# Optimization experiments

Hardware: AMD Instinct MI355X
Metric: run time of the kernel (lower is better)

Reference implementation:

```python
import jax, jax.numpy as jnp
import numpy as np

B, T, C, H, MAX_LEN = 16, 512, 1024, 16, 512
D = C // H  # head_dim = 64

def setup_inputs() -> dict:
    key = jax.random.key(0)
    ks = jax.random.split(key, 10)
    s = 1.0 / np.sqrt(C)
    return {
        "x": jax.random.normal(ks[0], (B, T, C), dtype=jnp.float32),
        "Wq": jax.random.normal(ks[1], (C, C), dtype=jnp.float32) * s,
        "bq": jnp.zeros((C,), dtype=jnp.float32),
        "Wk": jax.random.normal(ks[2], (C, C), dtype=jnp.float32) * s,
        "bk": jnp.zeros((C,), dtype=jnp.float32),
        "Wv": jax.random.normal(ks[3], (C, C), dtype=jnp.float32) * s,
        "bv": jnp.zeros((C,), dtype=jnp.float32),
        "Wo": jax.random.normal(ks[4], (C, C), dtype=jnp.float32) * s,
        "bo": jnp.zeros((C,), dtype=jnp.float32),
        "rel_pos_bias": jax.random.normal(ks[5], (H, MAX_LEN, MAX_LEN), dtype=jnp.float32) * 0.02,
    }

def reference(x, Wq, bq, Wk, bk, Wv, bv, Wo, bo, rel_pos_bias):
    scale = 1.0 / jnp.sqrt(jnp.float32(D))
    # projections (torch Linear: x @ W.T + b), reshape to (B,H,T,D)
    def proj(W, b):
        return (x @ W.T + b).reshape(B, T, H, D).transpose(0, 2, 1, 3)
    q, k, v = proj(Wq, bq), proj(Wk, bk), proj(Wv, bv)
    attn = jnp.einsum('bhtd,bhsd->bhts', q, k) * scale  # (B,H,T,T)
    attn = attn + rel_pos_bias[None, :, :T, :T]
    causal = jnp.triu(jnp.ones((T, T), dtype=bool), k=1)
    attn = jnp.where(causal[None, None], -jnp.inf, attn)
    attn = jax.nn.softmax(attn, axis=-1)  # dropout p=0 (eval) -> identity
    out = jnp.einsum('bhts,bhsd->bhtd', attn, v)
    out = out.transpose(0, 2, 1, 3).reshape(B, T, C)
    return out @ Wo.T + bo
```

## Files before the change

kernel.cpp:

```cpp
#include <hip/hip_runtime.h>
#include <stdint.h>
#include <math.h>

#define DEV static __device__ __forceinline__

typedef __attribute__((ext_vector_type(8))) __bf16 bf16x8;
typedef __attribute__((ext_vector_type(4))) float f32x4;
typedef unsigned short u16;

DEV u16 f2b(float f) {
  union { float f; uint32_t u; } x; x.f = f;
  uint32_t r = x.u + 0x7fffu + ((x.u >> 16) & 1u);
  return (u16)(r >> 16);
}

DEV uint32_t pk2(float a, float b) {
  return (uint32_t)f2b(a) | ((uint32_t)f2b(b) << 16);
}

DEV float b2f_lo(uint32_t u) { return __uint_as_float(u << 16); }
DEV float b2f_hi(uint32_t u) { return __uint_as_float(u & 0xffff0000u); }

DEV void glds16(const void* g, void* l) {
  __builtin_amdgcn_global_load_lds(
      (const __attribute__((address_space(1))) void*)g,
      (__attribute__((address_space(3))) void*)l, 16, 0, 0);
}

DEV f32x4 mfma16(bf16x8 a, bf16x8 b, f32x4 c) {
  return __builtin_amdgcn_mfma_f32_16x16x32_bf16(a, b, c, 0, 0, 0);
}

#define BAR() __builtin_amdgcn_s_barrier()
#define WAIT_LGKM()                                      \
  {                                                      \
    asm volatile("s_waitcnt lgkmcnt(0)" ::: "memory");   \
    __builtin_amdgcn_sched_barrier(0);                   \
  }
#define WAIT_VM3() asm volatile("s_waitcnt vmcnt(3)" ::: "memory")
#define WAIT_VM0() asm volatile("s_waitcnt vmcnt(0)" ::: "memory")

__global__ __launch_bounds__(256) void cvt_all(
    const float* __restrict__ x, const float* __restrict__ Wq,
    const float* __restrict__ Wk, const float* __restrict__ Wv,
    const float* __restrict__ Wo, const float* __restrict__ bias,
    u16* __restrict__ xb, u16* __restrict__ wqkv, u16* __restrict__ wo,
    u16* __restrict__ biasb) {
  size_t i = ((size_t)blockIdx.x * 256 + threadIdx.x) * 4;
  const float* s;
  u16* d;
  size_t off;
  float scale = 1.0f;
  if (i < 8388608)        { s = x;  d = xb;             off = i; }
  else if (i < 9437184)   { s = Wq; d = wqkv;           off = i - 8388608; }
  else if (i < 10485760)  { s = Wk; d = wqkv + 1048576; off = i - 9437184; }
  else if (i < 11534336)  { s = Wv; d = wqkv + 2097152; off = i - 10485760; }
  else if (i < 12582912)  { s = Wo; d = wo;             off = i - 11534336; }
  else { s = bias; d = biasb; off = i - 12582912; scale = 1.44269504f; }
  float4 v = *(const float4*)(s + off);
  ushort4 o;
  o.x = f2b(v.x * scale); o.y = f2b(v.y * scale);
  o.z = f2b(v.z * scale); o.w = f2b(v.w * scale);
  *(ushort4*)(d + off) = o;
}


DEV void stage_slot(const u16* A, const u16* Bw, int m0, int n0, int col,
                    int wave, int srow, int scol, u16* slotA, u16* slotB) {
  const u16* srcA = A + (size_t)(m0 + wave * 32 + srow) * 1024 + col + scol;
  glds16(srcA, slotA + wave * 1024);
  glds16(srcA + (size_t)16 * 1024, slotA + wave * 1024 + 512);
  glds16(Bw + (size_t)(n0 + wave * 16 + srow) * 1024 + col + scol,
         slotB + wave * 512);
}

DEV void load_frags(const u16* Rbase, const u16* Cbase, int wr, int wc,
                    int c16, int swz, bf16x8 rf[4], bf16x8 cf[4]) {
#pragma unroll
  for (int i = 0; i < 4; ++i)
    rf[i] = *(const bf16x8*)&Rbase[(wr * 64 + i * 16 + c16) * 32 + swz];
#pragma unroll
  for (int i = 0; i < 4; ++i)
    cf[i] = *(const bf16x8*)&Cbase[(wc * 64 + i * 16 + c16) * 32 + swz];
}

DEV void mfma_all(bf16x8 rf[4], bf16x8 cf[4], f32x4 acc[4][4]) {
#pragma unroll
  for (int i = 0; i < 4; ++i)
#pragma unroll
    for (int j = 0; j < 4; ++j) acc[i][j] = mfma16(rf[i], cf[j], acc[i][j]);
}

DEV void gemm_core(const u16* A, const u16* Bw, int m0, int n0, bool vblk,
                   int wave, int lane, u16 (*lsA)[8192], u16 (*lsB)[4096],
                   f32x4 acc[4][4]) {
  int q16 = lane >> 4, c16 = lane & 15;
  int wm = wave >> 1, wn = wave & 1;
  int wr = vblk ? wn : wm, wc = vblk ? wm : wn;
  int srow = lane >> 2;
  int scol = ((lane & 3) ^ ((lane >> 3) & 3)) * 8;
  int swz = (q16 ^ ((c16 >> 1) & 3)) * 8;

  stage_slot(A, Bw, m0, n0, 0, wave, srow, scol, lsA[0], lsB[0]);
  stage_slot(A, Bw, m0, n0, 32, wave, srow, scol, lsA[1], lsB[1]);
  WAIT_VM3();
  BAR();

#pragma unroll
  for (int g = 0; g < 32; ++g) {
    const int slot = g % 3;
    const u16* Rb = vblk ? &lsB[slot][0] : &lsA[slot][0];
    const u16* Cb = vblk ? &lsA[slot][0] : &lsB[slot][0];
    bf16x8 rf[4], cf[4];
    load_frags(Rb, Cb, wr, wc, c16, swz, rf, cf);
    if (g < 30)
      stage_slot(A, Bw, m0, n0, (g + 2) * 32, wave, srow, scol,
                 lsA[(g + 2) % 3], lsB[(g + 2) % 3]);
    BAR();
    WAIT_LGKM();
    __builtin_amdgcn_s_setprio(1);
    mfma_all(rf, cf, acc);
    __builtin_amdgcn_s_setprio(0);
    if (g < 30) { WAIT_VM3(); } else if (g == 30) { WAIT_VM0(); }
    BAR();
  }
}

__global__ __launch_bounds__(512, 4) void gemm_qkv(
    const u16* __restrict__ A, const u16* __restrict__ Bw,
    const float* __restrict__ bq, const float* __restrict__ bk,
    const float* __restrict__ bv,
    u16* __restrict__ qo, u16* __restrict__ ko, u16* __restrict__ vto) {
  __shared__ u16 lsA[3][8192];
  __shared__ u16 lsB[3][4096];
  int tid = threadIdx.x, wave = tid >> 6, lane = tid & 63;
  int q16 = lane >> 4, c16 = lane & 15;
  int m0 = blockIdx.y * 256, n0 = blockIdx.x * 128;
  int wm = wave >> 1, wn = wave & 1;
  const bool vblk = (n0 >= 2048);

  f32x4 acc[4][4];
#pragma unroll
  for (int i = 0; i < 4; ++i)
#pragma unroll
    for (int j = 0; j < 4; ++j) acc[i][j] = (f32x4)0.0f;

  gemm_core(A, Bw, m0, n0, vblk, wave, lane, lsA, lsB, acc);

  if (!vblk) {
#pragma unroll
    for (int mt = 0; mt < 4; ++mt) {
#pragma unroll
      for (int nt = 0; nt < 4; ++nt) {
        int n = n0 + wn * 64 + nt * 16 + c16;
        int which = n >> 10;
        int nl = n & 1023;
        int hh = nl >> 6, d = nl & 63;
        float bias = (which == 0 ? bq : bk)[nl];
        u16* dst = (which == 0 ? qo : ko);
#pragma unroll
        for (int r = 0; r < 4; ++r) {
          int m = m0 + wm * 64 + mt * 16 + q16 * 4 + r;
          int b = m >> 9, t = m & 511;
          size_t bh = (size_t)b * 16 + hh;
          dst[(bh * 512 + t) * 72 + d] = f2b(acc[mt][nt][r] + bias);
        }
      }
    }
  } else {
#pragma unroll
    for (int it = 0; it < 4; ++it) {
      int nbase = n0 + wn * 64 + it * 16 + q16 * 4;
      float4 bvv = *(const float4*)(bv + (nbase & 1023));
#pragma unroll
      for (int jt = 0; jt < 4; ++jt) {
        int m = m0 + wm * 64 + jt * 16 + c16;
        int b = m >> 9, t = m & 511;
        size_t bh4 = ((size_t)b * 16) * 4;
#pragma unroll
        for (int r = 0; r < 4; ++r) {
          int nl = (nbase + r) & 1023;
          int hh = nl >> 6, d = nl & 63;
          float bias = ((const float*)&bvv)[r];
          vto[((bh4 + (size_t)hh * 4 + (t >> 7)) * 64 + d) * 136 + (t & 127)] =
              f2b(acc[it][jt][r] + bias);
        }
      }
    }
  }
}

__global__ __launch_bounds__(256, 3) void attn_kernel(
    const u16* __restrict__ qglob, const u16* __restrict__ kglob,
    const u16* __restrict__ vtglob, const u16* __restrict__ biasb,
    u16* __restrict__ og) {
  __shared__ u16 lsK[128 * 72];
  __shared__ u16 lsV[64 * 136];
  __shared__ u16 lsP[4 * 32 * 72];

  int tid = threadIdx.x, wave = tid >> 6, lane = tid & 63;
  int q16 = lane >> 4, c16 = lane & 15;
  u16* lsPw = lsP + wave * (32 * 72);

  int p = blockIdx.x;
  int bx, bh, bx2 = -1, bh2 = 0;
  if (p < 256)      { bx = 3; bh = p; }
  else if (p < 512) { bx = 2; bh = p - 256; bx2 = 0; bh2 = p - 256; }
  else              { int q = p - 512; bx = 1; bh = 2 * q; bx2 = 1; bh2 = 2 * q + 1; }

  for (;;) {
    int b = bh >> 4, h = bh & 15;
    int q0 = bx * 128;

    const u16* qbase = qglob + (size_t)bh * (512 * 72) + (size_t)q0 * 72;
    const u16* kbase = kglob + (size_t)bh * (512 * 72);
    const u16* vbase = vtglob + (size_t)bh * 4 * (64 * 136);

    for (int i = wave; i < 18; i += 4)
      glds16(qbase + (size_t)i * 512 + lane * 8, lsK + i * 512);
    __syncthreads();
    bf16x8 qf[2][2];
#pragma unroll
    for (int nt = 0; nt < 2; ++nt)
#pragma unroll
      for (int ks = 0; ks < 2; ++ks)
        qf[nt][ks] = *(const bf16x8*)&lsK[(wave * 32 + nt * 16 + c16) * 72 +
                                          ks * 32 + q16 * 8];

    f32x4 oacc[2][4];
#pragma unroll
    for (int i = 0; i < 2; ++i)
#pragma unroll
      for (int j = 0; j < 4; ++j) oacc[i][j] = (f32x4)0.0f;
    float mold[2] = {-INFINITY, -INFINITY};
    float lsum[2] = {0.0f, 0.0f};
    const float SCL = 0.18033688f;

    for (int st = 0; st <= bx; ++st) {
      bool diag = (st == bx);
      __syncthreads();
      const u16* kt = kbase + (size_t)st * (128 * 72);
      for (int i = wave; i < 18; i += 4)
        glds16(kt + (size_t)i * 512 + lane * 8, lsK + i * 512);
      const u16* vt = vbase + (size_t)st * (64 * 136);
      for (int i = wave; i < 17; i += 4)
        glds16(vt + (size_t)i * 512 + lane * 8, lsV + i * 512);

      uint2 ub[2][8];
#pragma unroll
      for (int nt = 0; nt < 2; ++nt) {
        int qgl = q0 + wave * 32 + nt * 16 + c16;
        const u16* bp =
            biasb + ((size_t)h * 512 + qgl) * 512 + st * 128 + q16 * 4;
#pragma unroll
        for (int mt = 0; mt < 8; ++mt) ub[nt][mt] = *(const uint2*)(bp + mt * 16);
      }
      __syncthreads();

      f32x4 sa[8][2];
#pragma unroll
      for (int mt = 0; mt < 8; ++mt) {
        sa[mt][0] = (f32x4)0.0f;
        sa[mt][1] = (f32x4)0.0f;
      }
      int mtmax = diag ? 2 * wave + 2 : 8;
#pragma unroll
      for (int mt = 0; mt < 8; ++mt) {
        if (mt < mtmax) {
#pragma unroll
          for (int ks = 0; ks < 2; ++ks) {
            bf16x8 kf =
                *(const bf16x8*)&lsK[(mt * 16 + c16) * 72 + ks * 32 + q16 * 8];
            sa[mt][0] = mfma16(kf, qf[0][ks], sa[mt][0]);
            sa[mt][1] = mfma16(kf, qf[1][ks], sa[mt][1]);
          }
        }
      }

      float alpha[2];
#pragma unroll
      for (int nt = 0; nt < 2; ++nt) {
#pragma unroll
        for (int mt = 0; mt < 8; ++mt) {
          uint32_t lo = ub[nt][mt].x, hi = ub[nt][mt].y;
          f32x4 bv;
          bv[0] = b2f_lo(lo); bv[1] = b2f_hi(lo);
          bv[2] = b2f_lo(hi); bv[3] = b2f_hi(hi);
          sa[mt][nt] = sa[mt][nt] * SCL + bv;
        }
        if (diag) {
#pragma unroll
          for (int mt = 0; mt < 8; ++mt) {
            int d0 = mt * 16 + q16 * 4 - wave * 32 - nt * 16 - c16;
#pragma unroll
            for (int r = 0; r < 4; ++r)
              if (d0 + r > 0) sa[mt][nt][r] = -INFINITY;
          }
        }
        f32x4 m4 = sa[0][nt];
#pragma unroll
        for (int mt = 1; mt < 8; ++mt) {
          f32x4 v = sa[mt][nt];
          m4[0] = fmaxf(m4[0], v[0]); m4[1] = fmaxf(m4[1], v[1]);
          m4[2] = fmaxf(m4[2], v[2]); m4[3] = fmaxf(m4[3], v[3]);
        }
        float mx = fmaxf(fmaxf(m4[0], m4[1]), fmaxf(m4[2], m4[3]));
        mx = fmaxf(mx, __shfl_xor(mx, 16));
        mx = fmaxf(mx, __shfl_xor(mx, 32));
        float mnew = fmaxf(mold[nt], mx);
        alpha[nt] = exp2f(mold[nt] - mnew);
        mold[nt] = mnew;
        f32x4 s4 = (f32x4)0.0f;
#pragma unroll
        for (int mt = 0; mt < 8; ++mt) {
          f32x4 pq;
          pq[0] = exp2f(sa[mt][nt][0] - mnew);
          pq[1] = exp2f(sa[mt][nt][1] - mnew);
          pq[2] = exp2f(sa[mt][nt][2] - mnew);
          pq[3] = exp2f(sa[mt][nt][3] - mnew);
          sa[mt][nt] = pq;
          s4 += pq;
        }
        float ss = (s4[0] + s4[1]) + (s4[2] + s4[3]);
        ss += __shfl_xor(ss, 16);
        ss += __shfl_xor(ss, 32);
        lsum[nt] = lsum[nt] * alpha[nt] + ss;
      }

#pragma unroll
      for (int mo = 0; mo < 2; ++mo) {
        f32x4 av;
#pragma unroll
        for (int r = 0; r < 4; ++r) av[r] = __shfl(alpha[mo], q16 * 4 + r);
#pragma unroll
        for (int dt = 0; dt < 4; ++dt) oacc[mo][dt] *= av;
      }

      int G = diag ? wave + 1 : 4;
#pragma unroll
      for (int hf = 0; hf < 2; ++hf) {
        if (hf * 2 < G) {
#pragma unroll
          for (int nt = 0; nt < 2; ++nt)
#pragma unroll
            for (int mt4 = 0; mt4 < 4; ++mt4) {
              f32x4 pv = sa[hf * 4 + mt4][nt];
              uint2 w;
              w.x = pk2(pv[0], pv[1]);
              w.y = pk2(pv[2], pv[3]);
              *(uint2*)&lsPw[(nt * 16 + c16) * 72 + mt4 * 16 + q16 * 4] = w;
            }
#pragma unroll
          for (int ksh = 0; ksh < 2; ++ksh) {
            if (hf * 2 + ksh < G) {
              bf16x8 pf0 =
                  *(const bf16x8*)&lsPw[c16 * 72 + ksh * 32 + q16 * 8];
              bf16x8 pf1 =
                  *(const bf16x8*)&lsPw[(16 + c16) * 72 + ksh * 32 + q16 * 8];
#pragma unroll
              for (int dt = 0; dt < 4; ++dt) {
                bf16x8 vf = *(const bf16x8*)&lsV[(dt * 16 + c16) * 136 +
                                                 hf * 64 + ksh * 32 + q16 * 8];
                oacc[0][dt] = mfma16(pf0, vf, oacc[0][dt]);
                oacc[1][dt] = mfma16(pf1, vf, oacc[1][dt]);
              }
            }
          }
        }
      }
    }

#pragma unroll
    for (int mo = 0; mo < 2; ++mo) {
      f32x4 lv;
#pragma unroll
      for (int r = 0; r < 4; ++r) lv[r] = __shfl(lsum[mo], q16 * 4 + r);
#pragma unroll
      for (int r = 0; r < 4; ++r) {
        int tg = q0 + wave * 32 + mo * 16 + q16 * 4 + r;
        float inv = 1.0f / lv[r];
#pragma unroll
        for (int dt = 0; dt < 4; ++dt)
          og[((size_t)b * 512 + tg) * 1024 + h * 64 + dt * 16 + c16] =
              f2b(oacc[mo][dt][r] * inv);
      }
    }

    if (bx2 < 0) break;
    __syncthreads();
    bx = bx2; bh = bh2; bx2 = -1;
  }
}

__global__ __launch_bounds__(512, 4) void gemm_out(
    const u16* __restrict__ A, const u16* __restrict__ W,
    const float* __restrict__ bo, float* __restrict__ out) {
  __shared__ u16 lsA[3][8192];
  __shared__ u16 lsB[3][4096];
  int tid = threadIdx.x, wave = tid >> 6, lane = tid & 63;
  int q16 = lane >> 4, c16 = lane & 15;
  int m0 = blockIdx.y * 256, n0 = blockIdx.x * 128;
  int wm = wave >> 1, wn = wave & 1;

  f32x4 acc[4][4];
#pragma unroll
  for (int i = 0; i < 4; ++i)
#pragma unroll
    for (int j = 0; j < 4; ++j) acc[i][j] = (f32x4)0.0f;

  gemm_core(A, W, m0, n0, false, wave, lane, lsA, lsB, acc);

#pragma unroll
  for (int mt = 0; mt < 4; ++mt) {
#pragma unroll
    for (int nt = 0; nt < 4; ++nt) {
      int n = n0 + wn * 64 + nt * 16 + c16;
      float bias = bo[n];
#pragma unroll
      for (int r = 0; r < 4; ++r) {
        int m = m0 + wm * 64 + mt * 16 + q16 * 4 + r;
        out[(size_t)m * 1024 + n] = acc[mt][nt][r] + bias;
      }
    }
  }
}

extern "C" void kernel_launch(void* const* d_in, const int* in_sizes, int n_in,
                              void* d_out, int out_size, void* d_ws, size_t ws_size,
                              hipStream_t stream) {
  const float* x    = (const float*)d_in[0];
  const float* Wq   = (const float*)d_in[1];
  const float* bq   = (const float*)d_in[2];
  const float* Wk   = (const float*)d_in[3];
  const float* bk   = (const float*)d_in[4];
  const float* Wv   = (const float*)d_in[5];
  const float* bv   = (const float*)d_in[6];
  const float* Wo   = (const float*)d_in[7];
  const float* bo   = (const float*)d_in[8];
  const float* bias = (const float*)d_in[9];
  float* out = (float*)d_out;

  const size_t MB = 1u << 20;
  char* ws = (char*)d_ws;
  u16* xb    = (u16*)(ws);
  u16* wqkv  = (u16*)(ws + 16 * MB);
  u16* wo    = (u16*)(ws + 22 * MB);
  u16* biasb = (u16*)(ws + 24 * MB);
  u16* qb    = (u16*)(ws + 32 * MB);
  u16* kb    = (u16*)(ws + 50 * MB);
  u16* vtb   = (u16*)(ws + 68 * MB);
  u16* ab    = xb;

  cvt_all<<<16384, 256, 0, stream>>>(x, Wq, Wk, Wv, Wo, bias,
                                     xb, wqkv, wo, biasb);
  gemm_qkv<<<dim3(24, 32), 512, 0, stream>>>(xb, wqkv, bq, bk, bv, qb, kb, vtb);
  attn_kernel<<<dim3(640), 256, 0, stream>>>(qb, kb, vtb, biasb, ab);
  gemm_out<<<dim3(8, 32), 512, 0, stream>>>(ab, wo, bo, out);
}
```

Before: 269.1 us.

## Split attention query tile across eight waves of 16 rows each

Attention blocks grow from 4 to 8 waves, and each wave now owns 16 query rows instead of 32. Per-wave register state (scores, accumulators, bias loads) halves, and the causal diagonal tile is masked at finer granularity, so less MFMA work is wasted on masked entries. The per-wave P staging buffer shrinks and its row stride changes to 68. The cost is that each K/V fragment read from LDS is reused by only one query tile instead of two, which doubles LDS read traffic per unit of MFMA work.

```diff
diff --git a/kernel.cpp b/kernel.cpp
--- a/kernel.cpp
+++ b/kernel.cpp
@@ -190,17 +190,17 @@
   }
 }
 
-__global__ __launch_bounds__(256, 3) void attn_kernel(
+__global__ __launch_bounds__(512, 6) void attn_kernel(
     const u16* __restrict__ qglob, const u16* __restrict__ kglob,
     const u16* __restrict__ vtglob, const u16* __restrict__ biasb,
     u16* __restrict__ og) {
   __shared__ u16 lsK[128 * 72];
   __shared__ u16 lsV[64 * 136];
-  __shared__ u16 lsP[4 * 32 * 72];
+  __shared__ u16 lsP[8 * 16 * 68];
 
   int tid = threadIdx.x, wave = tid >> 6, lane = tid & 63;
   int q16 = lane >> 4, c16 = lane & 15;
-  u16* lsPw = lsP + wave * (32 * 72);
+  u16* lsPw = lsP + wave * (16 * 68);
 
   int p = blockIdx.x;
   int bx, bh, bx2 = -1, bh2 = 0;
@@ -216,54 +216,45 @@
     const u16* kbase = kglob + (size_t)bh * (512 * 72);
     const u16* vbase = vtglob + (size_t)bh * 4 * (64 * 136);
 
-    for (int i = wave; i < 18; i += 4)
+    for (int i = wave; i < 18; i += 8)
       glds16(qbase + (size_t)i * 512 + lane * 8, lsK + i * 512);
     __syncthreads();
-    bf16x8 qf[2][2];
-#pragma unroll
-    for (int nt = 0; nt < 2; ++nt)
-#pragma unroll
-      for (int ks = 0; ks < 2; ++ks)
-        qf[nt][ks] = *(const bf16x8*)&lsK[(wave * 32 + nt * 16 + c16) * 72 +
-                                          ks * 32 + q16 * 8];
-
-    f32x4 oacc[2][4];
-#pragma unroll
-    for (int i = 0; i < 2; ++i)
-#pragma unroll
-      for (int j = 0; j < 4; ++j) oacc[i][j] = (f32x4)0.0f;
-    float mold[2] = {-INFINITY, -INFINITY};
-    float lsum[2] = {0.0f, 0.0f};
+    bf16x8 qf[2];
+#pragma unroll
+    for (int ks = 0; ks < 2; ++ks)
+      qf[ks] = *(const bf16x8*)&lsK[(wave * 16 + c16) * 72 + ks * 32 + q16 * 8];
+
+    f32x4 oacc[4];
+#pragma unroll
+    for (int j = 0; j < 4; ++j) oacc[j] = (f32x4)0.0f;
+    float mold = -INFINITY;
+    float lsum = 0.0f;
     const float SCL = 0.18033688f;
 
     for (int st = 0; st <= bx; ++st) {
       bool diag = (st == bx);
       __syncthreads();
       const u16* kt = kbase + (size_t)st * (128 * 72);
-      for (int i = wave; i < 18; i += 4)
+      for (int i = wave; i < 18; i += 8)
         glds16(kt + (size_t)i * 512 + lane * 8, lsK + i * 512);
       const u16* vt = vbase + (size_t)st * (64 * 136);
-      for (int i = wave; i < 17; i += 4)
+      for (int i = wave; i < 17; i += 8)
         glds16(vt + (size_t)i * 512 + lane * 8, lsV + i * 512);
 
-      uint2 ub[2][8];
-#pragma unroll
-      for (int nt = 0; nt < 2; ++nt) {
-        int qgl = q0 + wave * 32 + nt * 16 + c16;
+      uint2 ub[8];
+      {
+        int qgl = q0 + wave * 16 + c16;
         const u16* bp =
             biasb + ((size_t)h * 512 + qgl) * 512 + st * 128 + q16 * 4;
 #pragma unroll
-        for (int mt = 0; mt < 8; ++mt) ub[nt][mt] = *(const uint2*)(bp + mt * 16);
+        for (int mt = 0; mt < 8; ++mt) ub[mt] = *(const uint2*)(bp + mt * 16);
       }
       __syncthreads();
 
-      f32x4 sa[8][2];
-#pragma unroll
-      for (int mt = 0; mt < 8; ++mt) {
-        sa[mt][0] = (f32x4)0.0f;
-        sa[mt][1] = (f32x4)0.0f;
-      }
-      int mtmax = diag ? 2 * wave + 2 : 8;
+      f32x4 sa[8];
+#pragma unroll
+      for (int mt = 0; mt < 8; ++mt) sa[mt] = (f32x4)0.0f;
+      int mtmax = diag ? wave + 1 : 8;
 #pragma unroll
       for (int mt = 0; mt < 8; ++mt) {
         if (mt < mtmax) {
@@ -271,98 +262,87 @@
           for (int ks = 0; ks < 2; ++ks) {
             bf16x8 kf =
                 *(const bf16x8*)&lsK[(mt * 16 + c16) * 72 + ks * 32 + q16 * 8];
-            sa[mt][0] = mfma16(kf, qf[0][ks], sa[mt][0]);
-            sa[mt][1] = mfma16(kf, qf[1][ks], sa[mt][1]);
+            sa[mt] = mfma16(kf, qf[ks], sa[mt]);
           }
         }
       }
 
-      float alpha[2];
-#pragma unroll
-      for (int nt = 0; nt < 2; ++nt) {
+#pragma unroll
+      for (int mt = 0; mt < 8; ++mt) {
+        uint32_t lo = ub[mt].x, hi = ub[mt].y;
+        f32x4 bv;
+        bv[0] = b2f_lo(lo); bv[1] = b2f_hi(lo);
+        bv[2] = b2f_lo(hi); bv[3] = b2f_hi(hi);
+        sa[mt] = sa[mt] * SCL + bv;
+      }
+      if (diag) {
 #pragma unroll
         for (int mt = 0; mt < 8; ++mt) {
-          uint32_t lo = ub[nt][mt].x, hi = ub[nt][mt].y;
-          f32x4 bv;
-          bv[0] = b2f_lo(lo); bv[1] = b2f_hi(lo);
-          bv[2] = b2f_lo(hi); bv[3] = b2f_hi(hi);
-          sa[mt][nt] = sa[mt][nt] * SCL + bv;
+          int d0 = mt * 16 + q16 * 4 - wave * 16 - c16;
+#pragma unroll
+          for (int r = 0; r < 4; ++r)
+            if (d0 + r > 0) sa[mt][r] = -INFINITY;
         }
-        if (diag) {
-#pragma unroll
-          for (int mt = 0; mt < 8; ++mt) {
-            int d0 = mt * 16 + q16 * 4 - wave * 32 - nt * 16 - c16;
-#pragma unroll
-            for (int r = 0; r < 4; ++r)
-              if (d0 + r > 0) sa[mt][nt][r] = -INFINITY;
-          }
-        }
-        f32x4 m4 = sa[0][nt];
-#pragma unroll
-        for (int mt = 1; mt < 8; ++mt) {
-          f32x4 v = sa[mt][nt];
-          m4[0] = fmaxf(m4[0], v[0]); m4[1] = fmaxf(m4[1], v[1]);
-          m4[2] = fmaxf(m4[2], v[2]); m4[3] = fmaxf(m4[3], v[3]);
-        }
-        float mx = fmaxf(fmaxf(m4[0], m4[1]), fmaxf(m4[2], m4[3]));
-        mx = fmaxf(mx, __shfl_xor(mx, 16));
-        mx = fmaxf(mx, __shfl_xor(mx, 32));
-        float mnew = fmaxf(mold[nt], mx);
-        alpha[nt] = exp2f(mold[nt] - mnew);
-        mold[nt] = mnew;
-        f32x4 s4 = (f32x4)0.0f;
-#pragma unroll
-        for (int mt = 0; mt < 8; ++mt) {
-          f32x4 pq;
-          pq[0] = exp2f(sa[mt][nt][0] - mnew);
-          pq[1] = exp2f(sa[mt][nt][1] - mnew);
-          pq[2] = exp2f(sa[mt][nt][2] - mnew);
-          pq[3] = exp2f(sa[mt][nt][3] - mnew);
-          sa[mt][nt] = pq;
-          s4 += pq;
-        }
-        float ss = (s4[0] + s4[1]) + (s4[2] + s4[3]);
-        ss += __shfl_xor(ss, 16);
-        ss += __shfl_xor(ss, 32);
-        lsum[nt] = lsum[nt] * alpha[nt] + ss;
-      }
-
-#pragma unroll
-      for (int mo = 0; mo < 2; ++mo) {
+      }
+      f32x4 m4 = sa[0];
+#pragma unroll
+      for (int mt = 1; mt < 8; ++mt) {
+        f32x4 v = sa[mt];
+        m4[0] = fmaxf(m4[0], v[0]); m4[1] = fmaxf(m4[1], v[1]);
+        m4[2] = fmaxf(m4[2], v[2]); m4[3] = fmaxf(m4[3], v[3]);
+      }
+      float mx = fmaxf(fmaxf(m4[0], m4[1]), fmaxf(m4[2], m4[3]));
+      mx = fmaxf(mx, __shfl_xor(mx, 16));
+      mx = fmaxf(mx, __shfl_xor(mx, 32));
+      float mnew = fmaxf(mold, mx);
+      float alpha = exp2f(mold - mnew);
+      mold = mnew;
+      f32x4 s4 = (f32x4)0.0f;
+#pragma unroll
+      for (int mt = 0; mt < 8; ++mt) {
+        f32x4 pq;
+        pq[0] = exp2f(sa[mt][0] - mnew);
+        pq[1] = exp2f(sa[mt][1] - mnew);
+        pq[2] = exp2f(sa[mt][2] - mnew);
+        pq[3] = exp2f(sa[mt][3] - mnew);
+        sa[mt] = pq;
+        s4 += pq;
+      }
+      float ss = (s4[0] + s4[1]) + (s4[2] + s4[3]);
+      ss += __shfl_xor(ss, 16);
+      ss += __shfl_xor(ss, 32);
+      lsum = lsum * alpha + ss;
+
+      {
         f32x4 av;
 #pragma unroll
-        for (int r = 0; r < 4; ++r) av[r] = __shfl(alpha[mo], q16 * 4 + r);
-#pragma unroll
-        for (int dt = 0; dt < 4; ++dt) oacc[mo][dt] *= av;
-      }
-
-      int G = diag ? wave + 1 : 4;
+        for (int r = 0; r < 4; ++r) av[r] = __shfl(alpha, q16 * 4 + r);
+#pragma unroll
+        for (int dt = 0; dt < 4; ++dt) oacc[dt] *= av;
+      }
+
+      int G = diag ? (wave >> 1) + 1 : 4;
 #pragma unroll
       for (int hf = 0; hf < 2; ++hf) {
         if (hf * 2 < G) {
 #pragma unroll
-          for (int nt = 0; nt < 2; ++nt)
-#pragma unroll
-            for (int mt4 = 0; mt4 < 4; ++mt4) {
-              f32x4 pv = sa[hf * 4 + mt4][nt];
-              uint2 w;
-              w.x = pk2(pv[0], pv[1]);
-              w.y = pk2(pv[2], pv[3]);
-              *(uint2*)&lsPw[(nt * 16 + c16) * 72 + mt4 * 16 + q16 * 4] = w;
-            }
+          for (int mt4 = 0; mt4 < 4; ++mt4) {
+            f32x4 pv = sa[hf * 4 + mt4];
+            uint2 w;
+            w.x = pk2(pv[0], pv[1]);
+            w.y = pk2(pv[2], pv[3]);
+            *(uint2*)&lsPw[c16 * 68 + mt4 * 16 + q16 * 4] = w;
+          }
 #pragma unroll
           for (int ksh = 0; ksh < 2; ++ksh) {
             if (hf * 2 + ksh < G) {
-              bf16x8 pf0 =
-                  *(const bf16x8*)&lsPw[c16 * 72 + ksh * 32 + q16 * 8];
-              bf16x8 pf1 =
-                  *(const bf16x8*)&lsPw[(16 + c16) * 72 + ksh * 32 + q16 * 8];
+              bf16x8 pf =
+                  *(const bf16x8*)&lsPw[c16 * 68 + ksh * 32 + q16 * 8];
 #pragma unroll
               for (int dt = 0; dt < 4; ++dt) {
                 bf16x8 vf = *(const bf16x8*)&lsV[(dt * 16 + c16) * 136 +
                                                  hf * 64 + ksh * 32 + q16 * 8];
-                oacc[0][dt] = mfma16(pf0, vf, oacc[0][dt]);
-                oacc[1][dt] = mfma16(pf1, vf, oacc[1][dt]);
+                oacc[dt] = mfma16(pf, vf, oacc[dt]);
               }
             }
           }
@@ -370,19 +350,18 @@
       }
     }
 
-#pragma unroll
-    for (int mo = 0; mo < 2; ++mo) {
+    {
       f32x4 lv;
 #pragma unroll
-      for (int r = 0; r < 4; ++r) lv[r] = __shfl(lsum[mo], q16 * 4 + r);
+      for (int r = 0; r < 4; ++r) lv[r] = __shfl(lsum, q16 * 4 + r);
 #pragma unroll
       for (int r = 0; r < 4; ++r) {
-        int tg = q0 + wave * 32 + mo * 16 + q16 * 4 + r;
+        int tg = q0 + wave * 16 + q16 * 4 + r;
         float inv = 1.0f / lv[r];
 #pragma unroll
         for (int dt = 0; dt < 4; ++dt)
           og[((size_t)b * 512 + tg) * 1024 + h * 64 + dt * 16 + c16] =
-              f2b(oacc[mo][dt][r] * inv);
+              f2b(oacc[dt][r] * inv);
       }
     }
 
@@ -454,6 +433,6 @@
   cvt_all<<<16384, 256, 0, stream>>>(x, Wq, Wk, Wv, Wo, bias,
                                      xb, wqkv, wo, biasb);
   gemm_qkv<<<dim3(24, 32), 512, 0, stream>>>(xb, wqkv, bq, bk, bv, qb, kb, vtb);
-  attn_kernel<<<dim3(640), 256, 0, stream>>>(qb, kb, vtb, biasb, ab);
+  attn_kernel<<<dim3(640), 512, 0, stream>>>(qb, kb, vtb, biasb, ab);
   gemm_out<<<dim3(8, 32), 512, 0, stream>>>(ab, wo, bo, out);
 }
```

Result: slower. 318.5 us (+18.3%).
